# Performance work log

Hardware: AMD Instinct MI355X
Metric: run time of the kernel (lower is better)

Reference implementation:

```python
import jax, jax.numpy as jnp
import numpy as np

B, T, C, H, W = 8, 10, 1, 64, 64
HID = 64

def conv2d_same(x, w):
    return jax.lax.conv_general_dilated(x, w, (1, 1), 'SAME', dimension_numbers=('NCHW', 'OIHW', 'NCHW'))

def setup_inputs():
    key = jax.random.key(0)
    ks = iter(jax.random.split(key, 32))
    inp = {'x': jax.random.uniform(next(ks), (B, T, C, H, W), jnp.float32)}
    def cell_params(prefix, in_ch):
        # 4 gates (i, f, g, o) stacked along output channels -> fused gate conv
        inp[prefix + '_Wx'] = jax.random.normal(next(ks), (4 * HID, in_ch, 3, 3), jnp.float32) * 0.05
        inp[prefix + '_Wh'] = jax.random.normal(next(ks), (4 * HID, HID, 3, 3), jnp.float32) * 0.05
        inp[prefix + '_Wc'] = jax.random.normal(next(ks), (4, HID, H, W), jnp.float32) * 0.05
        inp[prefix + '_b'] = jax.random.normal(next(ks), (4, HID, H, W), jnp.float32) * 0.05
    cell_params('enc0', C)
    cell_params('enc1', HID)
    cell_params('dec0', HID)
    cell_params('dec1', HID)
    inp['fin_w'] = jax.random.normal(next(ks), (1, HID, 3, 3), jnp.float32) * 0.05
    inp['fin_b'] = jnp.zeros((1,), jnp.float32)
    inp['prediction_len'] = 10
    return inp

def _cell(Wx, Wh, Wc, b, xt, h, c):
    # gate = act(W_x*x + W_h*h + W_c.c + bias); all 4 gates use the OLD (h, c)
    hid = h.shape[1]
    pre = conv2d_same(xt, Wx) + conv2d_same(h, Wh)  # (B, 4*hid, H, W)
    pre = pre.reshape(pre.shape[0], 4, hid, pre.shape[2], pre.shape[3])
    pre = pre + Wc[None] * c[:, None] + b[None]
    i = jax.nn.sigmoid(pre[:, 0])
    f = jax.nn.sigmoid(pre[:, 1])
    g = jnp.tanh(pre[:, 2])
    o = jax.nn.sigmoid(pre[:, 3])
    c_new = f * c + i * g
    h_new = o * jnp.tanh(c_new)
    return h_new, c_new

def reference(x, enc0_Wx, enc0_Wh, enc0_Wc, enc0_b, enc1_Wx, enc1_Wh, enc1_Wc, enc1_b, dec0_Wx, dec0_Wh, dec0_Wc, dec0_b, dec1_Wx, dec1_Wh, dec1_Wc, dec1_b, fin_w, fin_b, prediction_len):
    b_, t_ = x.shape[0], x.shape[1]
    h_, w_ = x.shape[3], x.shape[4]
    hid = enc0_Wc.shape[1]
    z = jnp.zeros((b_, hid, h_, w_), x.dtype)

    def enc_step(carry, xt):
        h0, c0, h1, c1 = carry
        h0, c0 = _cell(enc0_Wx, enc0_Wh, enc0_Wc, enc0_b, xt, h0, c0)
        h1, c1 = _cell(enc1_Wx, enc1_Wh, enc1_Wc, enc1_b, h0, h1, c1)
        return (h0, c0, h1, c1), None

    (eh0, ec0, eh1, ec1), _ = jax.lax.scan(enc_step, (z, z, z, z), jnp.swapaxes(x, 0, 1))
    state = eh1  # top-layer encoder hidden; decoder h/c start at zeros (as in torch code)

    def dec_step(carry, _):
        s, h0, c0, h1, c1 = carry
        h0, c0 = _cell(dec0_Wx, dec0_Wh, dec0_Wc, dec0_b, s, h0, c0)
        h1, c1 = _cell(dec1_Wx, dec1_Wh, dec1_Wc, dec1_b, h0, h1, c1)
        return (h1, h0, c0, h1, c1), h1

    _, ys = jax.lax.scan(dec_step, (state, z, z, z, z), None, length=prediction_len)
    # ys: (F, B, hid, H, W); Conv3d with (1,3,3) kernel == per-frame 2d conv
    f_ = ys.shape[0]
    y = ys.reshape(f_ * b_, hid, h_, w_)
    y = conv2d_same(y, fin_w) + fin_b[None, :, None, None]
    y = y.reshape(f_, b_, 1, h_, w_)
    return jax.nn.sigmoid(jnp.swapaxes(y, 0, 1))  # (B, F, 1, H, W)
```

## Files before the change

kernel.cpp:

```cpp
#include <hip/hip_runtime.h>
#include <hip/hip_bf16.h>
#include <math.h>

#define BSZ    8
#define TSTEPS 10
#define FLEN   10
#define HID    64
#define HW     4096
#define IMG    (HID * HW)
#define OC4    (4 * HID)
#define PADW   66
#define PPIX   (PADW * PADW)
#define PADIMG (PPIX * HID)
#define PADSZ  (BSZ * PADIMG)
#define SB     (BSZ * IMG)
#define KT_E0  640
#define KT_STD 1152

typedef __attribute__((ext_vector_type(8))) short bf16x8;
typedef __attribute__((ext_vector_type(4))) float f32x4;

__device__ __forceinline__ float sigmoidf_(float x) {
    return 1.0f / (1.0f + __expf(-x));
}
__device__ __forceinline__ float tanh_fast(float x) {
    float e = __expf(2.0f * x);
    return 1.0f - 2.0f / (e + 1.0f);
}
__device__ __forceinline__ float bf2f(short u) {
    union { unsigned u; float f; } cv;
    cv.u = ((unsigned)(unsigned short)u) << 16;
    return cv.f;
}
__device__ __forceinline__ short f2bf(float x) {
    __hip_bfloat16 h = __float2bfloat16(x);
    union { __hip_bfloat16 h; short s; } cv; cv.h = h;
    return cv.s;
}

__global__ __launch_bounds__(256) void reorder_w(
    const float* __restrict__ Wx, int icx,
    const float* __restrict__ Wh, __hip_bfloat16* __restrict__ Bw, int ktot) {
    int ocp = blockIdx.x, hid = ocp >> 2, gate = ocp & 3;
    int oc = gate * 64 + hid;
    for (int k = threadIdx.x; k < ktot; k += 256) {
        int c = k >> 6, j = k & 63;
        float v;
        if (icx == 1) {
            if (c == 0) v = (j < 9) ? Wx[oc * 9 + j] : 0.0f;
            else        v = Wh[(oc * 64 + j) * 9 + (c - 1)];
        } else {
            if (c < 9)  v = Wx[(oc * 64 + j) * 9 + c];
            else        v = Wh[(oc * 64 + j) * 9 + (c - 9)];
        }
        Bw[ocp * ktot + k] = __float2bfloat16(v);
    }
}

__global__ __launch_bounds__(256) void pack_wcb(
    const float* __restrict__ Wc, const float* __restrict__ bias,
    __hip_bfloat16* __restrict__ wcb) {
    int i = blockIdx.x * 256 + threadIdx.x;
    int hid = i >> 12, p = i & 4095;
    union { short s[8]; bf16x8 v; } u;
#pragma unroll
    for (int g = 0; g < 4; g++) {
        u.s[g]     = f2bf(Wc[(g * HID + hid) * HW + p]);
        u.s[4 + g] = f2bf(bias[(g * HID + hid) * HW + p]);
    }
    *(bf16x8*)&wcb[(size_t)i * 8] = u.v;
}

__global__ __launch_bounds__(256) void pack_x_all(
    const float* __restrict__ x, __hip_bfloat16* __restrict__ px_all) {
    int i = blockIdx.x * 256 + threadIdx.x;
    if (i >= TSTEPS * BSZ * PPIX) return;
    int t = i / (BSZ * PPIX);
    int rem = i - t * (BSZ * PPIX);
    int b = rem / PPIX;
    int pp = rem - b * PPIX;
    int y = pp / PADW, xx = pp - y * PADW;
    int oy = y - 1, ox = xx - 1;
    const float* xb = x + ((size_t)(b * TSTEPS + t)) * HW;
    bool interior = (oy >= 0 && oy < 64 && ox >= 0 && ox < 64);
    union { short s[16]; bf16x8 v[2]; } u;
#pragma unroll
    for (int tap = 0; tap < 9; tap++) {
        int yy = oy + tap / 3 - 1, xc = ox + tap % 3 - 1;
        float val = (interior && yy >= 0 && yy < 64 && xc >= 0 && xc < 64)
                        ? xb[yy * 64 + xc] : 0.0f;
        u.s[tap] = f2bf(val);
    }
#pragma unroll
    for (int tap = 9; tap < 16; tap++) u.s[tap] = 0;
    short* o = (short*)(px_all + (size_t)t * PADSZ + ((size_t)(b * PPIX + pp)) * HID);
    *(bf16x8*)&o[0] = u.v[0];
    *(bf16x8*)&o[8] = u.v[1];
}

struct CellArgs {
    const __hip_bfloat16* Bw;
    const __hip_bfloat16* src0;
    const __hip_bfloat16* src1;
    const __hip_bfloat16* wcb;
    float* cbuf;
    __hip_bfloat16* hout;
    int ktot;
    int n0;
    int first;
};

__global__ __launch_bounds__(256, 8) void gemm_cell_fused(CellArgs A0, CellArgs A1) {
    __shared__ short As[64 * 64];
    __shared__ short Bs[64 * 64];

    const bool z1 = (blockIdx.z != 0);
    const __hip_bfloat16* __restrict__ Bw   = z1 ? A1.Bw   : A0.Bw;
    const __hip_bfloat16* __restrict__ src0 = z1 ? A1.src0 : A0.src0;
    const __hip_bfloat16* __restrict__ src1 = z1 ? A1.src1 : A0.src1;
    const __hip_bfloat16* __restrict__ wcb  = z1 ? A1.wcb  : A0.wcb;
    float* __restrict__ cbuf                = z1 ? A1.cbuf : A0.cbuf;
    __hip_bfloat16* __restrict__ hout       = z1 ? A1.hout : A0.hout;
    const int ktot  = z1 ? A1.ktot  : A0.ktot;
    const int n0    = z1 ? A1.n0    : A0.n0;
    const int first = z1 ? A1.first : A0.first;

    const int tid  = threadIdx.x;
    const int lane = tid & 63;
    const int wave = tid >> 6;
    const int quad = lane >> 4;
    const int l15  = lane & 15;
    const int wr = wave >> 1;
    const int wc = wave & 1;
    const int px0 = blockIdx.x * 64;
    const int oc0 = blockIdx.y * 64;

    int a_off[2], s_off[2];
#pragma unroll
    for (int it = 0; it < 2; it++) {
        int idx = it * 256 + tid;
        int rr = idx >> 3, seg = idx & 7;
        int segx = seg ^ (rr & 7);
        a_off[it] = (oc0 + rr) * ktot + segx * 8;
        int px = px0 + rr;
        int b = px >> 12, p = px & 4095, y = p >> 6, x = p & 63;
        s_off[it] = ((b * PADW + y + 1) * PADW + (x + 1)) * HID + segx * 8;
    }
    const int ldsbase = (tid & ~63) * 8;
    const int xa = l15 & 7;

    f32x4 acc[2][2] = {};
    const int nchunks = n0 + 9;

    for (int kk = 0; kk < nchunks; kk++) {
        const __hip_bfloat16* src;
        int tap;
        if (kk < n0) { src = src0; tap = (n0 == 1) ? 4 : kk; }
        else         { src = src1; tap = kk - n0; }
        int dd = ((tap / 3) - 1) * (PADW * HID) + ((tap % 3) - 1) * HID;
        int ka = kk * 64;
#pragma unroll
        for (int it = 0; it < 2; it++) {
            __builtin_amdgcn_global_load_lds(
                (const __attribute__((address_space(1))) void*)(Bw + a_off[it] + ka),
                (__attribute__((address_space(3))) void*)(&As[it * 2048 + ldsbase]),
                16, 0, 0);
            __builtin_amdgcn_global_load_lds(
                (const __attribute__((address_space(1))) void*)(src + s_off[it] + dd),
                (__attribute__((address_space(3))) void*)(&Bs[it * 2048 + ldsbase]),
                16, 0, 0);
        }
        __syncthreads();
#pragma unroll
        for (int k2 = 0; k2 < 2; k2++) {
            int sA = ((k2 * 4 + quad) ^ xa) * 8;
            bf16x8 af[2], bfr[2];
#pragma unroll
            for (int i = 0; i < 2; i++)
                af[i] = *(const bf16x8*)&As[(wr * 32 + i * 16 + l15) * 64 + sA];
#pragma unroll
            for (int j = 0; j < 2; j++)
                bfr[j] = *(const bf16x8*)&Bs[(wc * 32 + j * 16 + l15) * 64 + sA];
#pragma unroll
            for (int i = 0; i < 2; i++)
#pragma unroll
                for (int j = 0; j < 2; j++)
                    acc[i][j] = __builtin_amdgcn_mfma_f32_16x16x32_bf16(
                        af[i], bfr[j], acc[i][j], 0, 0, 0);
        }
        __syncthreads();
    }

    short* hl = As;
    const int hid0 = oc0 >> 2;
#pragma unroll
    for (int i = 0; i < 2; i++) {
        int hidl = wr * 8 + i * 4 + quad;
        int hid = hid0 + hidl;
#pragma unroll
        for (int j = 0; j < 2; j++) {
            int pxl = wc * 32 + j * 16 + l15;
            int px = px0 + pxl;
            int b = px >> 12, p = px & 4095;
            size_t ci = ((size_t)(b * HID + hid)) * HW + p;
            float cv = first ? 0.0f : cbuf[ci];
            bf16x8 wv = *(const bf16x8*)&wcb[((size_t)hid * HW + p) * 8];
            float pg[4];
#pragma unroll
            for (int r = 0; r < 4; r++)
                pg[r] = acc[i][j][r] + bf2f(wv[r]) * cv + bf2f(wv[4 + r]);
            float ig = sigmoidf_(pg[0]);
            float fg = sigmoidf_(pg[1]);
            float gg = tanh_fast(pg[2]);
            float og = sigmoidf_(pg[3]);
            float cn = fg * cv + ig * gg;
            cbuf[ci] = cn;
            float hn = og * tanh_fast(cn);
            hl[pxl * 40 + hidl] = f2bf(hn);
        }
    }
    __syncthreads();
    if (tid < 128) {
        int pxl = tid >> 1, q = tid & 1;
        bf16x8 v = *(const bf16x8*)&hl[pxl * 40 + q * 8];
        int px = px0 + pxl;
        int b = px >> 12, p = px & 4095, y = p >> 6, x = p & 63;
        *(bf16x8*)&hout[((size_t)((b * PADW + y + 1) * PADW + (x + 1))) * HID
                        + hid0 + q * 8] = v;
    }
}

__global__ __launch_bounds__(256) void final_conv(
    const __hip_bfloat16* __restrict__ ph, const float* __restrict__ fw,
    const float* __restrict__ fb, float* __restrict__ out, int f) {
    int b = blockIdx.y;
    int p = blockIdx.x * 256 + threadIdx.x;
    int y = p >> 6, x = p & 63;
    float acc = fb[0];
#pragma unroll
    for (int tap = 0; tap < 9; tap++) {
        const bf16x8* base = (const bf16x8*)(
            ph + ((b * PADW + y + (tap / 3)) * PADW + (x + (tap % 3))) * HID);
#pragma unroll
        for (int c8 = 0; c8 < 8; c8++) {
            bf16x8 v = base[c8];
#pragma unroll
            for (int jj = 0; jj < 8; jj++)
                acc = fmaf(bf2f(v[jj]), fw[(c8 * 8 + jj) * 9 + tap], acc);
        }
    }
    out[((size_t)(b * FLEN + f)) * HW + p] = sigmoidf_(acc);
}

extern "C" void kernel_launch(void* const* d_in, const int* in_sizes, int n_in,
                              void* d_out, int out_size, void* d_ws, size_t ws_size,
                              hipStream_t stream) {
    const float* x = (const float*)d_in[0];
    const float* Wx_[4] = {(const float*)d_in[1], (const float*)d_in[5],
                           (const float*)d_in[9], (const float*)d_in[13]};
    const float* Wh_[4] = {(const float*)d_in[2], (const float*)d_in[6],
                           (const float*)d_in[10], (const float*)d_in[14]};
    const float* Wc_[4] = {(const float*)d_in[3], (const float*)d_in[7],
                           (const float*)d_in[11], (const float*)d_in[15]};
    const float* b_[4]  = {(const float*)d_in[4], (const float*)d_in[8],
                           (const float*)d_in[12], (const float*)d_in[16]};
    const float* fin_w  = (const float*)d_in[17];
    const float* fin_b  = (const float*)d_in[18];
    float* out = (float*)d_out;

    char* wsb = (char*)d_ws;
    const size_t H_BYTES  = 8ull * PADSZ * sizeof(short);
    const size_t PX_BYTES = 10ull * PADSZ * sizeof(short);
    const size_t C_BYTES  = 4ull * SB * sizeof(float);
    const size_t WCB_ELEM = (size_t)HID * HW * 8;

    __hip_bfloat16* hb = (__hip_bfloat16*)wsb;
    __hip_bfloat16* px_all = (__hip_bfloat16*)(wsb + H_BYTES);
    float* cbuf = (float*)(wsb + H_BYTES + PX_BYTES);
    __hip_bfloat16* wcb = (__hip_bfloat16*)(wsb + H_BYTES + PX_BYTES + C_BYTES);
    __hip_bfloat16* bw = wcb + 4 * WCB_ELEM;

    __hip_bfloat16* e0buf[2] = {hb + 0 * (size_t)PADSZ, hb + 1 * (size_t)PADSZ};
    __hip_bfloat16* e1buf[2] = {hb + 2 * (size_t)PADSZ, hb + 3 * (size_t)PADSZ};
    __hip_bfloat16* d0buf[2] = {hb + 4 * (size_t)PADSZ, hb + 5 * (size_t)PADSZ};
    __hip_bfloat16* d1buf[2] = {hb + 6 * (size_t)PADSZ, hb + 7 * (size_t)PADSZ};

    float* ec0 = cbuf + 0 * (size_t)SB;
    float* ec1 = cbuf + 1 * (size_t)SB;
    float* dc0 = cbuf + 2 * (size_t)SB;
    float* dc1 = cbuf + 3 * (size_t)SB;

    __hip_bfloat16* wcb_[4] = {wcb, wcb + WCB_ELEM, wcb + 2 * WCB_ELEM, wcb + 3 * WCB_ELEM};
    __hip_bfloat16* bw_e0 = bw;
    __hip_bfloat16* bw_e1 = bw_e0 + (size_t)OC4 * KT_E0;
    __hip_bfloat16* bw_d0 = bw_e1 + (size_t)OC4 * KT_STD;
    __hip_bfloat16* bw_d1 = bw_d0 + (size_t)OC4 * KT_STD;
    __hip_bfloat16* bw_[4] = {bw_e0, bw_e1, bw_d0, bw_d1};
    float* c_[4] = {ec0, ec1, dc0, dc1};

    hipMemsetAsync(wsb, 0, H_BYTES, stream);

    reorder_w<<<dim3(OC4), 256, 0, stream>>>(Wx_[0], 1,   Wh_[0], bw_e0, KT_E0);
    reorder_w<<<dim3(OC4), 256, 0, stream>>>(Wx_[1], HID, Wh_[1], bw_e1, KT_STD);
    reorder_w<<<dim3(OC4), 256, 0, stream>>>(Wx_[2], HID, Wh_[2], bw_d0, KT_STD);
    reorder_w<<<dim3(OC4), 256, 0, stream>>>(Wx_[3], HID, Wh_[3], bw_d1, KT_STD);
    for (int cix = 0; cix < 4; cix++)
        pack_wcb<<<dim3((HID * HW) / 256), 256, 0, stream>>>(Wc_[cix], b_[cix], wcb_[cix]);
    pack_x_all<<<dim3((TSTEPS * BSZ * PPIX + 255) / 256), 256, 0, stream>>>(x, px_all);

    auto cellargs = [&](int cell, const __hip_bfloat16* s0, const __hip_bfloat16* s1,
                        __hip_bfloat16* ho, int kt, int nn0, int fi) {
        CellArgs a;
        a.Bw = bw_[cell]; a.src0 = s0; a.src1 = s1; a.wcb = wcb_[cell];
        a.cbuf = c_[cell]; a.hout = ho; a.ktot = kt; a.n0 = nn0; a.first = fi;
        return a;
    };
    auto px = [&](int t) { return px_all + (size_t)t * PADSZ; };

    dim3 gfin(16, BSZ);

    {
        CellArgs a = cellargs(0, px(0), e0buf[1], e0buf[0], KT_E0, 1, 1);
        gemm_cell_fused<<<dim3(512, 4, 1), 256, 0, stream>>>(a, a);
    }
    for (int k = 1; k <= 9; k++) {
        int t0 = k, t1 = k - 1;
        CellArgs a0 = cellargs(0, px(t0), e0buf[(t0 - 1) & 1], e0buf[t0 & 1],
                               KT_E0, 1, 0);
        CellArgs a1 = cellargs(1, e0buf[t1 & 1], e1buf[(t1 - 1) & 1], e1buf[t1 & 1],
                               KT_STD, 9, (t1 == 0) ? 1 : 0);
        gemm_cell_fused<<<dim3(512, 4, 2), 256, 0, stream>>>(a0, a1);
    }
    {
        CellArgs a = cellargs(1, e0buf[1], e1buf[0], e1buf[1], KT_STD, 9, 0);
        gemm_cell_fused<<<dim3(512, 4, 1), 256, 0, stream>>>(a, a);
    }
    __hip_bfloat16* enc_top = e1buf[1];

    for (int f = 0; f < FLEN; f++) {
        const __hip_bfloat16* s = (f == 0) ? enc_top : d1buf[(f - 1) & 1];
        CellArgs a0 = cellargs(2, s, d0buf[(f - 1) & 1], d0buf[f & 1],
                               KT_STD, 9, (f == 0) ? 1 : 0);
        gemm_cell_fused<<<dim3(512, 4, 1), 256, 0, stream>>>(a0, a0);
        CellArgs a1 = cellargs(3, d0buf[f & 1], d1buf[(f - 1) & 1], d1buf[f & 1],
                               KT_STD, 9, (f == 0) ? 1 : 0);
        gemm_cell_fused<<<dim3(512, 4, 1), 256, 0, stream>>>(a1, a1);
        final_conv<<<gfin, 256, 0, stream>>>(d1buf[f & 1], fin_w, fin_b, out, f);
    }
}
```

Before: 1.505 ms.

## Stage padded halo rows in LDS once and reuse across all nine conv taps

Each block now covers two image rows (128 pixels) and stages the padded 4x66x64 input halo into LDS once per source, then runs all nine taps from it by shifting LDS offsets. Before, a fresh 64x64 tile was loaded per tap through LDS. Weights are now read straight from global into registers instead of through LDS. This cuts repeated activation traffic and barriers per tap, but makes weight loads uncached by LDS, halves the grid and raises register and LDS use (launch bounds drop to 4 blocks).

```diff
diff --git a/kernel.cpp b/kernel.cpp
--- a/kernel.cpp
+++ b/kernel.cpp
@@ -110,9 +110,8 @@
     int first;
 };
 
-__global__ __launch_bounds__(256, 8) void gemm_cell_fused(CellArgs A0, CellArgs A1) {
-    __shared__ short As[64 * 64];
-    __shared__ short Bs[64 * 64];
+__global__ __launch_bounds__(256, 4) void gemm_cell_fused(CellArgs A0, CellArgs A1) {
+    __shared__ short halo[4 * PADW * HID];
 
     const bool z1 = (blockIdx.z != 0);
     const __hip_bfloat16* __restrict__ Bw   = z1 ? A1.Bw   : A0.Bw;
@@ -132,76 +131,93 @@
     const int l15  = lane & 15;
     const int wr = wave >> 1;
     const int wc = wave & 1;
-    const int px0 = blockIdx.x * 64;
+    const int px0 = blockIdx.x * 128;
     const int oc0 = blockIdx.y * 64;
-
-    int a_off[2], s_off[2];
-#pragma unroll
-    for (int it = 0; it < 2; it++) {
-        int idx = it * 256 + tid;
-        int rr = idx >> 3, seg = idx & 7;
-        int segx = seg ^ (rr & 7);
-        a_off[it] = (oc0 + rr) * ktot + segx * 8;
-        int px = px0 + rr;
-        int b = px >> 12, p = px & 4095, y = p >> 6, x = p & 63;
-        s_off[it] = ((b * PADW + y + 1) * PADW + (x + 1)) * HID + segx * 8;
-    }
-    const int ldsbase = (tid & ~63) * 8;
-    const int xa = l15 & 7;
-
-    f32x4 acc[2][2] = {};
-    const int nchunks = n0 + 9;
-
-    for (int kk = 0; kk < nchunks; kk++) {
-        const __hip_bfloat16* src;
-        int tap;
-        if (kk < n0) { src = src0; tap = (n0 == 1) ? 4 : kk; }
-        else         { src = src1; tap = kk - n0; }
-        int dd = ((tap / 3) - 1) * (PADW * HID) + ((tap % 3) - 1) * HID;
-        int ka = kk * 64;
-#pragma unroll
-        for (int it = 0; it < 2; it++) {
-            __builtin_amdgcn_global_load_lds(
-                (const __attribute__((address_space(1))) void*)(Bw + a_off[it] + ka),
-                (__attribute__((address_space(3))) void*)(&As[it * 2048 + ldsbase]),
-                16, 0, 0);
-            __builtin_amdgcn_global_load_lds(
-                (const __attribute__((address_space(1))) void*)(src + s_off[it] + dd),
-                (__attribute__((address_space(3))) void*)(&Bs[it * 2048 + ldsbase]),
-                16, 0, 0);
-        }
-        __syncthreads();
+    const int b    = px0 >> 12;
+    const int ybase = (px0 & 4095) >> 6;
+
+    int arow[2];
+#pragma unroll
+    for (int i = 0; i < 2; i++)
+        arow[i] = (oc0 + wr * 32 + i * 16 + l15) * ktot;
+
+    const size_t gbase = (size_t)(b * PADW + ybase) * PADW * HID;
+    auto stage_halo = [&](const __hip_bfloat16* src) {
+#pragma unroll
+        for (int it = 0; it < 9; it++) {
+            int idx = it * 256 + tid;
+            if (idx < 2112) {
+                int p = idx >> 3, sg = idx & 7;
+                int sgx = sg ^ (p & 7);
+                __builtin_amdgcn_global_load_lds(
+                    (const __attribute__((address_space(1))) void*)(
+                        src + gbase + (size_t)p * HID + sgx * 8),
+                    (__attribute__((address_space(3))) void*)(&halo[idx * 8]),
+                    16, 0, 0);
+            }
+        }
+    };
+
+    f32x4 acc[2][4] = {};
+
+    auto chunk = [&](int ak, int ty, int tx) {
+        bf16x8 a_[2][2];
+#pragma unroll
+        for (int i = 0; i < 2; i++)
+#pragma unroll
+            for (int k2 = 0; k2 < 2; k2++)
+                a_[i][k2] = *(const bf16x8*)&Bw[arow[i] + ak * 64 + k2 * 32 + quad * 8];
 #pragma unroll
         for (int k2 = 0; k2 < 2; k2++) {
-            int sA = ((k2 * 4 + quad) ^ xa) * 8;
-            bf16x8 af[2], bfr[2];
+            bf16x8 bfr[4];
+#pragma unroll
+            for (int j = 0; j < 4; j++) {
+                int ph_ = (wc + ty) * PADW + j * 16 + l15 + tx;
+                int sl  = ((k2 * 4 + quad) ^ (ph_ & 7)) * 8;
+                bfr[j] = *(const bf16x8*)&halo[ph_ * HID + sl];
+            }
 #pragma unroll
             for (int i = 0; i < 2; i++)
-                af[i] = *(const bf16x8*)&As[(wr * 32 + i * 16 + l15) * 64 + sA];
-#pragma unroll
-            for (int j = 0; j < 2; j++)
-                bfr[j] = *(const bf16x8*)&Bs[(wc * 32 + j * 16 + l15) * 64 + sA];
-#pragma unroll
-            for (int i = 0; i < 2; i++)
-#pragma unroll
-                for (int j = 0; j < 2; j++)
+#pragma unroll
+                for (int j = 0; j < 4; j++)
                     acc[i][j] = __builtin_amdgcn_mfma_f32_16x16x32_bf16(
-                        af[i], bfr[j], acc[i][j], 0, 0, 0);
-        }
-        __syncthreads();
-    }
-
-    short* hl = As;
+                        a_[i][k2], bfr[j], acc[i][j], 0, 0, 0);
+        }
+    };
+
+    stage_halo(src0);
+    __syncthreads();
+    if (n0 == 1) {
+        chunk(0, 1, 1);
+    } else {
+#pragma unroll
+        for (int ty = 0; ty < 3; ty++)
+#pragma unroll
+            for (int tx = 0; tx < 3; tx++)
+                chunk(ty * 3 + tx, ty, tx);
+    }
+    __syncthreads();
+
+    stage_halo(src1);
+    __syncthreads();
+#pragma unroll
+    for (int ty = 0; ty < 3; ty++)
+#pragma unroll
+        for (int tx = 0; tx < 3; tx++)
+            chunk(n0 + ty * 3 + tx, ty, tx);
+    __syncthreads();
+
+    short* hl = halo;
     const int hid0 = oc0 >> 2;
 #pragma unroll
     for (int i = 0; i < 2; i++) {
         int hidl = wr * 8 + i * 4 + quad;
         int hid = hid0 + hidl;
 #pragma unroll
-        for (int j = 0; j < 2; j++) {
-            int pxl = wc * 32 + j * 16 + l15;
+        for (int j = 0; j < 4; j++) {
+            int pxl = wc * 64 + j * 16 + l15;
             int px = px0 + pxl;
-            int b = px >> 12, p = px & 4095;
+            int p = px & 4095;
             size_t ci = ((size_t)(b * HID + hid)) * HW + p;
             float cv = first ? 0.0f : cbuf[ci];
             bf16x8 wv = *(const bf16x8*)&wcb[((size_t)hid * HW + p) * 8];
@@ -220,11 +236,11 @@
         }
     }
     __syncthreads();
-    if (tid < 128) {
+    {
         int pxl = tid >> 1, q = tid & 1;
         bf16x8 v = *(const bf16x8*)&hl[pxl * 40 + q * 8];
         int px = px0 + pxl;
-        int b = px >> 12, p = px & 4095, y = p >> 6, x = p & 63;
+        int p = px & 4095, y = p >> 6, x = p & 63;
         *(bf16x8*)&hout[((size_t)((b * PADW + y + 1) * PADW + (x + 1))) * HID
                         + hid0 + q * 8] = v;
     }
@@ -321,7 +337,7 @@
 
     {
         CellArgs a = cellargs(0, px(0), e0buf[1], e0buf[0], KT_E0, 1, 1);
-        gemm_cell_fused<<<dim3(512, 4, 1), 256, 0, stream>>>(a, a);
+        gemm_cell_fused<<<dim3(256, 4, 1), 256, 0, stream>>>(a, a);
     }
     for (int k = 1; k <= 9; k++) {
         int t0 = k, t1 = k - 1;
@@ -329,11 +345,11 @@
                                KT_E0, 1, 0);
         CellArgs a1 = cellargs(1, e0buf[t1 & 1], e1buf[(t1 - 1) & 1], e1buf[t1 & 1],
                                KT_STD, 9, (t1 == 0) ? 1 : 0);
-        gemm_cell_fused<<<dim3(512, 4, 2), 256, 0, stream>>>(a0, a1);
+        gemm_cell_fused<<<dim3(256, 4, 2), 256, 0, stream>>>(a0, a1);
     }
     {
         CellArgs a = cellargs(1, e0buf[1], e1buf[0], e1buf[1], KT_STD, 9, 0);
-        gemm_cell_fused<<<dim3(512, 4, 1), 256, 0, stream>>>(a, a);
+        gemm_cell_fused<<<dim3(256, 4, 1), 256, 0, stream>>>(a, a);
     }
     __hip_bfloat16* enc_top = e1buf[1];
 
@@ -341,10 +357,10 @@
         const __hip_bfloat16* s = (f == 0) ? enc_top : d1buf[(f - 1) & 1];
         CellArgs a0 = cellargs(2, s, d0buf[(f - 1) & 1], d0buf[f & 1],
                                KT_STD, 9, (f == 0) ? 1 : 0);
-        gemm_cell_fused<<<dim3(512, 4, 1), 256, 0, stream>>>(a0, a0);
+        gemm_cell_fused<<<dim3(256, 4, 1), 256, 0, stream>>>(a0, a0);
         CellArgs a1 = cellargs(3, d0buf[f & 1], d1buf[(f - 1) & 1], d1buf[f & 1],
                                KT_STD, 9, (f == 0) ? 1 : 0);
-        gemm_cell_fused<<<dim3(512, 4, 1), 256, 0, stream>>>(a1, a1);
+        gemm_cell_fused<<<dim3(256, 4, 1), 256, 0, stream>>>(a1, a1);
         final_conv<<<gfin, 256, 0, stream>>>(d1buf[f & 1], fin_w, fin_b, out, f);
     }
 }
```

Measured after the change: 1.912 ms. 1.27x slower.
